# Optimization experiments

Hardware: AMD Instinct MI355X
Metric: run time of the kernel (lower is better)

Reference implementation:

```python
import jax, jax.numpy as jnp
import numpy as np

SUB_TRAJECTORY_LENGTH = 4096
INHERENT_NEIGHBORHOOD = 0.5

def setup_inputs() -> dict:
    key = jax.random.key(0)
    predictions = jax.random.normal(key, (64, 8192, 64), dtype=jnp.float32)
    return {"predictions": predictions, "start_timestamp": 2048}

def reference(predictions, start_timestamp):
    # predictions: [B, T, D]; sum over window [s, s+L) of ||p[:, j+1] - p[:, j]||^2
    s = start_timestamp  # static Python int
    L = SUB_TRAJECTORY_LENGTH
    diff = predictions[:, s + 1 : s + L + 1] - predictions[:, s : s + L]  # [B, L, D]
    batch_size = predictions.shape[0]
    loss = jnp.sum(diff * diff) / batch_size - INHERENT_NEIGHBORHOOD
    return loss
```

## Files before the change

kernel.cpp:

```cpp
#include <hip/hip_runtime.h>


#define BATCH 64
#define TDIM  8192
#define DDIM  64
#define LWIN  4096

#define D4    16
#define TD4   (TDIM * D4)

#define RCHAIN 8
#define NTHREADS 256
#define NCHAINS  (LWIN / RCHAIN)
#define TOTTHR   (BATCH * D4 * NCHAINS)
#define NBLOCKS  (TOTTHR / NTHREADS)

__global__ __launch_bounds__(NTHREADS) void nl_partial_kernel(
    const float4* __restrict__ pred, const int* __restrict__ s_ptr,
    float* __restrict__ partial) {
    const int s   = *s_ptr;
    const int tid = blockIdx.x * NTHREADS + threadIdx.x;
    const int c    = tid & 15;
    const int g    = tid >> 4;
    const int jblk = g & (NCHAINS - 1);
    const int b    = g >> 9;

    const float4* p = pred + ((size_t)b * TD4 + (size_t)(s + jblk * RCHAIN) * D4 + c);

    float4 a[RCHAIN + 1];
    #pragma unroll
    for (int i = 0; i <= RCHAIN; ++i) a[i] = p[i * D4];

    float acc = 0.0f;
    #pragma unroll
    for (int i = 0; i < RCHAIN; ++i) {
        const float dx = a[i + 1].x - a[i].x;
        const float dy = a[i + 1].y - a[i].y;
        const float dz = a[i + 1].z - a[i].z;
        const float dw = a[i + 1].w - a[i].w;
        acc += dx * dx + dy * dy + dz * dz + dw * dw;
    }

    #pragma unroll
    for (int off = 32; off > 0; off >>= 1) acc += __shfl_down(acc, off, 64);

    __shared__ float smem[NTHREADS / 64];
    const int lane = threadIdx.x & 63;
    const int wid  = threadIdx.x >> 6;
    if (lane == 0) smem[wid] = acc;
    __syncthreads();
    if (threadIdx.x == 0)
        partial[blockIdx.x] = smem[0] + smem[1] + smem[2] + smem[3];
}

__global__ __launch_bounds__(NTHREADS) void nl_final_kernel(
    const float* __restrict__ partial, float* __restrict__ out) {
    float acc = 0.0f;
    #pragma unroll
    for (int i = 0; i < NBLOCKS / NTHREADS; ++i)
        acc += partial[threadIdx.x + i * NTHREADS];

    #pragma unroll
    for (int off = 32; off > 0; off >>= 1) acc += __shfl_down(acc, off, 64);

    __shared__ float smem[NTHREADS / 64];
    const int lane = threadIdx.x & 63;
    const int wid  = threadIdx.x >> 6;
    if (lane == 0) smem[wid] = acc;
    __syncthreads();
    if (threadIdx.x == 0) {
        const float total = smem[0] + smem[1] + smem[2] + smem[3];
        out[0] = total * (1.0f / BATCH) - 0.5f;
    }
}

extern "C" void kernel_launch(void* const* d_in, const int* in_sizes, int n_in,
                              void* d_out, int out_size, void* d_ws, size_t ws_size,
                              hipStream_t stream) {
    const float4* pred = (const float4*)d_in[0];
    const int* s_ptr   = (const int*)d_in[1];
    float* out         = (float*)d_out;
    float* partial     = (float*)d_ws;

    nl_partial_kernel<<<NBLOCKS, NTHREADS, 0, stream>>>(pred, s_ptr, partial);
    nl_final_kernel<<<1, NTHREADS, 0, stream>>>(partial, out);
}
```

Before: 17.60 us.

## Fuse final reduction into main kernel via packed fixed-point atomic counter

Drops the separate single-block final-reduction kernel. Each block now converts its partial sum to 2^20-scaled fixed point and adds it, together with a block count in the top 12 bits, to one 64-bit device atomic. The block that sees the count reach NBLOCKS writes the scaled result and resets the accumulator. This removes a second launch and the partial-sum round trip through memory. In exchange it adds 2048 same-address atomics and a small fixed-point truncation error per block.

```diff
diff --git a/kernel.cpp b/kernel.cpp
--- a/kernel.cpp
+++ b/kernel.cpp
@@ -9,15 +9,21 @@
 #define D4    16
 #define TD4   (TDIM * D4)
 
-#define RCHAIN 8
+#define RCHAIN   8
 #define NTHREADS 256
 #define NCHAINS  (LWIN / RCHAIN)
 #define TOTTHR   (BATCH * D4 * NCHAINS)
 #define NBLOCKS  (TOTTHR / NTHREADS)
 
-__global__ __launch_bounds__(NTHREADS) void nl_partial_kernel(
+__device__ unsigned long long nl_acc = 0ULL;
+
+#define CNT_SHIFT 52
+#define SUM_MASK  ((1ULL << CNT_SHIFT) - 1ULL)
+#define FIX_SCALE 1048576.0
+
+__global__ __launch_bounds__(NTHREADS) void nl_fused_kernel(
     const float4* __restrict__ pred, const int* __restrict__ s_ptr,
-    float* __restrict__ partial) {
+    float* __restrict__ out) {
     const int s   = *s_ptr;
     const int tid = blockIdx.x * NTHREADS + threadIdx.x;
     const int c    = tid & 15;
@@ -49,28 +55,18 @@
     const int wid  = threadIdx.x >> 6;
     if (lane == 0) smem[wid] = acc;
     __syncthreads();
-    if (threadIdx.x == 0)
-        partial[blockIdx.x] = smem[0] + smem[1] + smem[2] + smem[3];
-}
 
-__global__ __launch_bounds__(NTHREADS) void nl_final_kernel(
-    const float* __restrict__ partial, float* __restrict__ out) {
-    float acc = 0.0f;
-    #pragma unroll
-    for (int i = 0; i < NBLOCKS / NTHREADS; ++i)
-        acc += partial[threadIdx.x + i * NTHREADS];
-
-    #pragma unroll
-    for (int off = 32; off > 0; off >>= 1) acc += __shfl_down(acc, off, 64);
-
-    __shared__ float smem[NTHREADS / 64];
-    const int lane = threadIdx.x & 63;
-    const int wid  = threadIdx.x >> 6;
-    if (lane == 0) smem[wid] = acc;
-    __syncthreads();
     if (threadIdx.x == 0) {
-        const float total = smem[0] + smem[1] + smem[2] + smem[3];
-        out[0] = total * (1.0f / BATCH) - 0.5f;
+        const float bs = smem[0] + smem[1] + smem[2] + smem[3];
+        const unsigned long long contrib =
+            (1ULL << CNT_SHIFT) | (unsigned long long)((double)bs * FIX_SCALE);
+        const unsigned long long old = atomicAdd(&nl_acc, contrib);
+        const unsigned long long newv = old + contrib;
+        if ((newv >> CNT_SHIFT) == (unsigned long long)NBLOCKS) {
+            const double total = (double)(newv & SUM_MASK) * (1.0 / FIX_SCALE);
+            out[0] = (float)(total * (1.0 / BATCH) - 0.5);
+            atomicExch(&nl_acc, 0ULL);
+        }
     }
 }
 
@@ -80,8 +76,6 @@
     const float4* pred = (const float4*)d_in[0];
     const int* s_ptr   = (const int*)d_in[1];
     float* out         = (float*)d_out;
-    float* partial     = (float*)d_ws;
 
-    nl_partial_kernel<<<NBLOCKS, NTHREADS, 0, stream>>>(pred, s_ptr, partial);
-    nl_final_kernel<<<1, NTHREADS, 0, stream>>>(partial, out);
+    nl_fused_kernel<<<NBLOCKS, NTHREADS, 0, stream>>>(pred, s_ptr, out);
 }
```

New measurement: 34.48 us. 1.96x slower.
